# Kernel tuning notes

Hardware: AMD Instinct MI355X
Metric: run time of the kernel (lower is better)

The kernel has to match this reference:

```python
import jax, jax.numpy as jnp
import numpy as np

P = 64       # number of pathways
NV = 512     # features per pathway (nvar[i])
W = 256      # hidden width per pathway
COV = 16     # covariates
B = 2048     # batch
EPS = 1e-5   # BatchNorm eps
SLOPE = 0.2  # LeakyReLU negative slope


def _lrelu(v):
    return jnp.where(v >= 0, v, SLOPE * v)


def setup_inputs() -> dict:
    key = jax.random.key(0)
    ks = jax.random.split(key, 8)
    x = jax.random.normal(ks[0], (B, P * NV + COV), dtype=jnp.float32)
    # per-pathway weights (no bias), stacked across pathways -> grouped GEMM
    W1 = jax.random.normal(ks[1], (P, NV, W), dtype=jnp.float32) * (1.0 / np.sqrt(NV))
    W2 = jax.random.normal(ks[2], (P, W, W), dtype=jnp.float32) * (1.0 / np.sqrt(W))
    W3 = jax.random.normal(ks[3], (P, W), dtype=jnp.float32) * (1.0 / np.sqrt(W))
    gamma = jnp.ones((P,), dtype=jnp.float32)   # bn_path weight
    beta = jnp.zeros((P,), dtype=jnp.float32)   # bn_path bias
    fc_w = jax.random.normal(ks[4], (P + COV, 1), dtype=jnp.float32) * 0.05
    fc_b = jnp.full((1,), 0.001, dtype=jnp.float32)
    return {"x": x, "W1": W1, "W2": W2, "W3": W3,
            "gamma": gamma, "beta": beta, "fc_w": fc_w, "fc_b": fc_b}


def reference(x, W1, W2, W3, gamma, beta, fc_w, fc_b):
    # pathway blocks (dropout = identity in eval): grouped GEMMs over P pathways
    xp = x[:, : P * NV].reshape(B, P, NV)
    h = _lrelu(jnp.einsum('bpi,pio->bpo', xp, W1))
    h = _lrelu(jnp.einsum('bpi,pio->bpo', h, W2))
    p = _lrelu(jnp.einsum('bpi,pi->bp', h, W3))          # [B, P]
    # BatchNorm1d (training-mode batch statistics, biased variance)
    mean = p.mean(axis=0)
    var = p.var(axis=0)
    pn = (p - mean) / jnp.sqrt(var + EPS) * gamma + beta
    # global L2 (Frobenius) normalization, as torch.norm(pathway_layer, 2)
    pn = pn / jnp.linalg.norm(pn)
    # concat covariates, final linear + sigmoid
    z = jnp.concatenate([pn, x[:, P * NV: P * NV + COV]], axis=1)  # [B, P+COV]
    return jax.nn.sigmoid(z @ fc_w + fc_b)                         # [B, 1]
```

## Files before the change

### kernel.cpp

```cpp
#include <hip/hip_runtime.h>
#include <hip/hip_bf16.h>

#define PW 64
#define NV 512
#define HW 256
#define COV 16
#define BATCH 2048
#define XROW (PW * NV + COV)
#define IMG 16384
#define IMG2 8192

typedef short s16x8 __attribute__((ext_vector_type(8)));
typedef float f32x4 __attribute__((ext_vector_type(4)));

__device__ __forceinline__ unsigned short f2bf(float f) {
    union { float f; unsigned int u; } v;
    v.f = f;
    unsigned int u = v.u;
    unsigned int r = (u + 0x7fffu + ((u >> 16) & 1u)) >> 16;
    return (unsigned short)r;
}

__device__ __forceinline__ unsigned int pack2(float a, float b) {
    __hip_bfloat162 h = __float22bfloat162_rn(float2{a, b});
    union { __hip_bfloat162 h; unsigned int u; } c;
    c.h = h;
    return c.u;
}

__device__ __forceinline__ float lrelu(float v) { return v >= 0.f ? v : 0.2f * v; }

__device__ __forceinline__ void gl_lds16(const void* g, void* l) {
    __builtin_amdgcn_global_load_lds(
        (const __attribute__((address_space(1))) void*)g,
        (__attribute__((address_space(3))) void*)l, 16, 0, 0);
}

#define WAITV(n) asm volatile("s_waitcnt vmcnt(" #n ") lgkmcnt(0)" ::: "memory")
#define BAR()    __builtin_amdgcn_s_barrier()
#define SCHED0() __builtin_amdgcn_sched_barrier(0)

__global__ __launch_bounds__(256)
void transpose_all(const float* __restrict__ W1, const float* __restrict__ W2,
                   unsigned short* __restrict__ W1I, unsigned short* __restrict__ W2I) {
    __shared__ float tile[64][260];
    int bx = blockIdx.x;
    const int t = threadIdx.x;
    const bool isW1 = bx < 512;
    const float* src;
    if (isW1) {
        int p = bx >> 3, kb = bx & 7;
        src = W1 + ((size_t)p * NV + kb * 64) * HW;
    } else {
        int b2 = bx - 512;
        int p = b2 >> 2, kb64 = b2 & 3;
        src = W2 + ((size_t)p * HW + kb64 * 64) * HW;
    }
    #pragma unroll
    for (int i = 0; i < 16; ++i) {
        int idx = t + i * 256;
        int r = idx >> 6, c4 = (idx & 63) << 2;
        *(float4*)&tile[r][c4] = *(const float4*)(src + (size_t)r * HW + c4);
    }
    __syncthreads();
    if (isW1) {
        int p = bx >> 3, kb = bx & 7;
        unsigned short* dst = W1I + (size_t)(p * 8 + kb) * IMG;
        #pragma unroll
        for (int pass = 0; pass < 8; ++pass) {
            int idx = pass * 256 + t;
            int n = idx >> 3, s = idx & 7;
            int g = s ^ (n & 7);
            unsigned short v[8];
            #pragma unroll
            for (int j = 0; j < 8; ++j)
                v[j] = f2bf(tile[g * 8 + j][n]);
            *(s16x8*)(dst + (size_t)idx * 8) = *(s16x8*)v;
        }
    } else {
        int b2 = bx - 512;
        int p = b2 >> 2, kb64 = b2 & 3;
        unsigned short* dst = W2I + (size_t)(p * 8 + kb64 * 2) * IMG2;
        #pragma unroll
        for (int pass = 0; pass < 8; ++pass) {
            int idx = pass * 256 + t;
            int h = idx >> 10;
            int rem = idx & 1023;
            int n = rem >> 2, s = rem & 3;
            int g = s ^ ((n >> 1) & 3);
            int krow = h * 32 + g * 8;
            unsigned short v[8];
            #pragma unroll
            for (int j = 0; j < 8; ++j)
                v[j] = f2bf(tile[krow + j][n]);
            *(s16x8*)(dst + (size_t)h * IMG2 + n * 32 + s * 8) = *(s16x8*)v;
        }
    }
}

__global__ __launch_bounds__(256, 2)
void pathway_fused(const float* __restrict__ x, const unsigned short* __restrict__ W1I,
                   const unsigned short* __restrict__ W2I, const float* __restrict__ W3,
                   float* __restrict__ pvec) {
    __shared__ __align__(16) unsigned short lds[40960];

    const int lin = blockIdx.x;
    const int xcd = lin & 7;
    const int idx = lin >> 3;
    const int p   = xcd * 8 + (idx >> 5);
    const int m   = idx & 31;
    const int bm0 = m * 64;

    const int t = threadIdx.x;
    const int lane = t & 63;
    const int wave = t >> 6;
    const int wn   = wave * 64;
    const int l15  = lane & 15;
    const int quad = lane >> 4;

    const float* Ap          = x   + (size_t)p * NV;
    const unsigned short* B1 = W1I + (size_t)p * 8 * IMG;
    const unsigned short* B2 = W2I + (size_t)p * 8 * IMG2;

    int arow[4], aoff[4];
    #pragma unroll
    for (int i = 0; i < 4; ++i) {
        int ii = t + i * 256;
        arow[i] = ii >> 4;
        int acol = (ii & 15) * 4;
        int slot = (acol >> 3) ^ (arow[i] & 7);
        aoff[i] = arow[i] * 64 + slot * 8 + (acol & 7);
    }
    int acolc[4];
    #pragma unroll
    for (int i = 0; i < 4; ++i) acolc[i] = ((t + i * 256) & 15) * 4;

    float4 S0[4], S1[4];
    f32x4 acc[4][4] = {};

#define XLOAD(dst, k0) { \
    _Pragma("unroll") \
    for (int i = 0; i < 4; ++i) \
        dst[i] = *(const float4*)(Ap + (size_t)(bm0 + arow[i]) * XROW + (k0) + acolc[i]); }

#define APACK(src, buf) { \
    unsigned short* Asb = lds + 32768 + (buf) * 4096; \
    _Pragma("unroll") \
    for (int i = 0; i < 4; ++i) { \
        uint2 u; \
        u.x = pack2(src[i].x, src[i].y); \
        u.y = pack2(src[i].z, src[i].w); \
        *(uint2*)&Asb[aoff[i]] = u; } }

#define B1STAGE(buf, kb) { \
    const unsigned short* img = B1 + (size_t)(kb) * IMG; \
    _Pragma("unroll") \
    for (int c = 0; c < 8; ++c) { \
        int off = wave * 8192 + c * 1024; \
        gl_lds16((const char*)img + off + lane * 16, (char*)lds + (buf) * 32768 + off); } }

#define MFMA_A(buf) { \
    const unsigned short* Asb = lds + 32768 + (buf) * 4096; \
    const unsigned short* Bsb = lds + (buf) * 16384; \
    __builtin_amdgcn_s_setprio(1); \
    _Pragma("unroll") \
    for (int kk = 0; kk < 64; kk += 32) { \
        s16x8 af[4], bfr[4]; \
        _Pragma("unroll") \
        for (int mi = 0; mi < 4; ++mi) { \
            int row = mi * 16 + l15; \
            int slot = ((kk >> 3) + quad) ^ (row & 7); \
            af[mi] = *(const s16x8*)&Asb[row * 64 + slot * 8]; } \
        _Pragma("unroll") \
        for (int ni = 0; ni < 4; ++ni) { \
            int row = wn + ni * 16 + l15; \
            int slot = ((kk >> 3) + quad) ^ (row & 7); \
            bfr[ni] = *(const s16x8*)&Bsb[row * 64 + slot * 8]; } \
        _Pragma("unroll") \
        for (int mi = 0; mi < 4; ++mi) \
            _Pragma("unroll") \
            for (int ni = 0; ni < 4; ++ni) \
                acc[mi][ni] = __builtin_amdgcn_mfma_f32_16x16x32_bf16( \
                    af[mi], bfr[ni], acc[mi][ni], 0, 0, 0); } \
    __builtin_amdgcn_s_setprio(0); }

#define W2STAGE(buf, kb) { \
    const unsigned short* img = B2 + (size_t)(kb) * IMG2; \
    _Pragma("unroll") \
    for (int c = 0; c < 4; ++c) { \
        int off = wave * 4096 + c * 1024; \
        gl_lds16((const char*)img + off + lane * 16, (char*)lds + 16384 + (buf) * 8192 + off); } }

#define MFMA_B(buf, kb) { \
    const unsigned short* W2b = lds + 16384 + (buf) * 8192; \
    __builtin_amdgcn_s_setprio(1); \
    { \
        s16x8 af[4], bfr[4]; \
        _Pragma("unroll") \
        for (int mi = 0; mi < 4; ++mi) { \
            int row = mi * 16 + l15; \
            int slot = ((kb) * 4 + quad) ^ (row & 7); \
            af[mi] = *(const s16x8*)&lds[row * 256 + slot * 8]; } \
        _Pragma("unroll") \
        for (int ni = 0; ni < 4; ++ni) { \
            int row = wn + ni * 16 + l15; \
            int slot = quad ^ ((row >> 1) & 3); \
            bfr[ni] = *(const s16x8*)&W2b[row * 32 + slot * 8]; } \
        _Pragma("unroll") \
        for (int mi = 0; mi < 4; ++mi) \
            _Pragma("unroll") \
            for (int ni = 0; ni < 4; ++ni) \
                acc[mi][ni] = __builtin_amdgcn_mfma_f32_16x16x32_bf16( \
                    af[mi], bfr[ni], acc[mi][ni], 0, 0, 0); \
    } \
    __builtin_amdgcn_s_setprio(0); }

#define STEP_A(tt, sLoad, sPack, WN) { \
    if ((tt) + 1 < 8) B1STAGE(1 - ((tt) & 1), (tt) + 1); \
    SCHED0(); \
    if ((tt) + 2 < 8) XLOAD(sLoad, ((tt) + 2) * 64); \
    if ((tt) + 1 < 8) APACK(sPack, 1 - ((tt) & 1)); \
    MFMA_A((tt) & 1); \
    WAITV(WN); \
    BAR(); \
    SCHED0(); }

#define STEP_B(tt, WN) { \
    if ((tt) + 2 < 8) W2STAGE(((tt) + 2) % 3, (tt) + 2); \
    SCHED0(); \
    MFMA_B((tt) % 3, (tt)); \
    WAITV(WN); \
    BAR(); \
    SCHED0(); }

    XLOAD(S0, 0);
    SCHED0();
    B1STAGE(0, 0);
    SCHED0();
    XLOAD(S1, 64);
    APACK(S0, 0);
    WAITV(4);
    BAR();
    SCHED0();

    STEP_A(0, S0, S1, 4);
    STEP_A(1, S1, S0, 4);
    STEP_A(2, S0, S1, 4);
    STEP_A(3, S1, S0, 4);
    STEP_A(4, S0, S1, 4);
    STEP_A(5, S1, S0, 4);
    STEP_A(6, S0, S1, 0);
    STEP_A(7, S1, S0, 0);

    W2STAGE(0, 0);
    SCHED0();
    W2STAGE(1, 1);
    #pragma unroll
    for (int mi = 0; mi < 4; ++mi)
        #pragma unroll
        for (int ni = 0; ni < 4; ++ni)
            #pragma unroll
            for (int r = 0; r < 4; ++r) {
                int row = mi * 16 + quad * 4 + r;
                int col = wn + ni * 16 + l15;
                int slot = (col >> 3) ^ (row & 7);
                lds[row * 256 + slot * 8 + (col & 7)] = f2bf(lrelu(acc[mi][ni][r]));
            }
    WAITV(4);
    BAR();
    SCHED0();

    #pragma unroll
    for (int mi = 0; mi < 4; ++mi)
        #pragma unroll
        for (int ni = 0; ni < 4; ++ni)
            acc[mi][ni] = (f32x4){0.f, 0.f, 0.f, 0.f};

    STEP_B(0, 4);
    STEP_B(1, 4);
    STEP_B(2, 4);
    STEP_B(3, 4);
    STEP_B(4, 4);
    STEP_B(5, 4);
    STEP_B(6, 0);
    STEP_B(7, 0);

    float* red = (float*)(lds + 16384);
    float w3v[4];
    #pragma unroll
    for (int ni = 0; ni < 4; ++ni)
        w3v[ni] = W3[(size_t)p * HW + wn + ni * 16 + l15];
    float part[4][4];
    #pragma unroll
    for (int mi = 0; mi < 4; ++mi) {
        #pragma unroll
        for (int r = 0; r < 4; ++r) {
            float s = 0.f;
            #pragma unroll
            for (int ni = 0; ni < 4; ++ni)
                s += lrelu(acc[mi][ni][r]) * w3v[ni];
            part[mi][r] = s;
        }
    }
    #pragma unroll
    for (int off = 1; off < 16; off <<= 1)
        #pragma unroll
        for (int mi = 0; mi < 4; ++mi)
            #pragma unroll
            for (int r = 0; r < 4; ++r)
                part[mi][r] += __shfl_xor(part[mi][r], off);
    if (l15 == 0)
        #pragma unroll
        for (int mi = 0; mi < 4; ++mi)
            #pragma unroll
            for (int r = 0; r < 4; ++r)
                red[wave * 64 + mi * 16 + quad * 4 + r] = part[mi][r];
    __syncthreads();
    if (t < 64) {
        float s = red[0 * 64 + t] + red[1 * 64 + t] + red[2 * 64 + t] + red[3 * 64 + t];
        pvec[(size_t)p * BATCH + bm0 + t] = lrelu(s);
    }
#undef XLOAD
#undef APACK
#undef B1STAGE
#undef MFMA_A
#undef W2STAGE
#undef MFMA_B
#undef STEP_A
#undef STEP_B
}

__global__ __launch_bounds__(256)
void stats_k(const float* __restrict__ pvec, float* __restrict__ stat) {
    const int p = blockIdx.x;
    float s = 0.f, q = 0.f;
    for (int i = threadIdx.x; i < BATCH; i += 256) {
        float v = pvec[(size_t)p * BATCH + i];
        s += v; q += v * v;
    }
    #pragma unroll
    for (int off = 32; off; off >>= 1) {
        s += __shfl_down(s, off);
        q += __shfl_down(q, off);
    }
    __shared__ float ls[4], lq[4];
    const int wave = threadIdx.x >> 6, lane = threadIdx.x & 63;
    if (lane == 0) { ls[wave] = s; lq[wave] = q; }
    __syncthreads();
    if (threadIdx.x == 0) {
        float S = ls[0] + ls[1] + ls[2] + ls[3];
        float Q = lq[0] + lq[1] + lq[2] + lq[3];
        float mean = S * (1.f / BATCH);
        float var  = Q * (1.f / BATCH) - mean * mean;
        stat[p]       = mean;
        stat[64 + p]  = rsqrtf(var + 1e-5f);
        stat[128 + p] = var;
    }
}

__global__ __launch_bounds__(256)
void final_k(const float* __restrict__ pvec, const float* __restrict__ stat,
             const float* __restrict__ gamma, const float* __restrict__ beta,
             const float* __restrict__ x, const float* __restrict__ fc_w,
             const float* __restrict__ fc_b, float* __restrict__ out) {
    const int b = blockIdx.x * 256 + threadIdx.x;
    float nsq = 0.f;
    #pragma unroll
    for (int p = 0; p < PW; ++p) {
        float g = gamma[p], bt = beta[p], var = stat[128 + p], inv = stat[64 + p];
        nsq += (float)BATCH * (g * g * var * inv * inv + bt * bt);
    }
    const float rn = rsqrtf(nsq);
    float acc = fc_b[0];
    #pragma unroll
    for (int p = 0; p < PW; ++p) {
        float pn = (pvec[(size_t)p * BATCH + b] - stat[p]) * stat[64 + p] * gamma[p] + beta[p];
        acc += pn * rn * fc_w[p];
    }
    #pragma unroll
    for (int c = 0; c < COV; ++c)
        acc += x[(size_t)b * XROW + PW * NV + c] * fc_w[PW + c];
    out[b] = 1.f / (1.f + __expf(-acc));
}

extern "C" void kernel_launch(void* const* d_in, const int* in_sizes, int n_in,
                              void* d_out, int out_size, void* d_ws, size_t ws_size,
                              hipStream_t stream) {
    const float* x     = (const float*)d_in[0];
    const float* W1    = (const float*)d_in[1];
    const float* W2    = (const float*)d_in[2];
    const float* W3    = (const float*)d_in[3];
    const float* gamma = (const float*)d_in[4];
    const float* beta  = (const float*)d_in[5];
    const float* fc_w  = (const float*)d_in[6];
    const float* fc_b  = (const float*)d_in[7];
    float* out = (float*)d_out;

    char* ws = (char*)d_ws;
    size_t off = 0;
    unsigned short* W1I = (unsigned short*)(ws + off); off += (size_t)PW * NV * HW * 2;
    unsigned short* W2I = (unsigned short*)(ws + off); off += (size_t)PW * HW * HW * 2;
    float* pvec = (float*)(ws + off); off += (size_t)PW * BATCH * 4;
    float* stat = (float*)(ws + off); off += 256 * 4;

    transpose_all<<<dim3(512 + 256), 256, 0, stream>>>(W1, W2, W1I, W2I);
    pathway_fused<<<dim3(2048), 256, 0, stream>>>(x, W1I, W2I, W3, pvec);
    stats_k<<<PW, 256, 0, stream>>>(pvec, stat);
    final_k<<<BATCH / 256, 256, 0, stream>>>(pvec, stat, gamma, beta, x, fc_w, fc_b, out);
}
```

Baseline: 481.1 us.

## Enlarge pathway block tile to 256 batch rows with eight waves

Each block of the fused pathway kernel now covers 256 batch rows with 512 threads arranged as 2x4 waves, instead of 64 rows with 4 waves. Every staged W1/W2 tile is reused across four times as many rows, cutting weight traffic into LDS by a factor of four, and the grid shrinks to 512 blocks. LDS use grows to about 160KB, which limits residency to one block per CU. The W2 pipeline also drops from triple to double buffering with a full wait each step, which may expose more load latency.

```diff
diff --git a/kernel.cpp b/kernel.cpp
--- a/kernel.cpp
+++ b/kernel.cpp
@@ -98,23 +98,24 @@
     }
 }
 
-__global__ __launch_bounds__(256, 2)
+__global__ __launch_bounds__(512, 2)
 void pathway_fused(const float* __restrict__ x, const unsigned short* __restrict__ W1I,
                    const unsigned short* __restrict__ W2I, const float* __restrict__ W3,
                    float* __restrict__ pvec) {
-    __shared__ __align__(16) unsigned short lds[40960];
+    __shared__ __align__(16) unsigned short lds[81920];
 
     const int lin = blockIdx.x;
     const int xcd = lin & 7;
     const int idx = lin >> 3;
-    const int p   = xcd * 8 + (idx >> 5);
-    const int m   = idx & 31;
-    const int bm0 = m * 64;
+    const int p   = xcd * 8 + (idx >> 3);
+    const int mt  = idx & 7;
+    const int bm0 = mt * 256;
 
     const int t = threadIdx.x;
     const int lane = t & 63;
     const int wave = t >> 6;
-    const int wn   = wave * 64;
+    const int wm   = wave >> 2;
+    const int wn   = wave & 3;
     const int l15  = lane & 15;
     const int quad = lane >> 4;
 
@@ -122,62 +123,60 @@
     const unsigned short* B1 = W1I + (size_t)p * 8 * IMG;
     const unsigned short* B2 = W2I + (size_t)p * 8 * IMG2;
 
-    int arow[4], aoff[4];
-    #pragma unroll
-    for (int i = 0; i < 4; ++i) {
-        int ii = t + i * 256;
-        arow[i] = ii >> 4;
-        int acol = (ii & 15) * 4;
-        int slot = (acol >> 3) ^ (arow[i] & 7);
-        aoff[i] = arow[i] * 64 + slot * 8 + (acol & 7);
-    }
-    int acolc[4];
-    #pragma unroll
-    for (int i = 0; i < 4; ++i) acolc[i] = ((t + i * 256) & 15) * 4;
-
-    float4 S0[4], S1[4];
-    f32x4 acc[4][4] = {};
-
-#define XLOAD(dst, k0) { \
+    int arow[8], acolc[8], aoff[8];
+    #pragma unroll
+    for (int i = 0; i < 8; ++i) {
+        int ii = t + i * 512;
+        arow[i]  = ii >> 4;
+        acolc[i] = (ii & 15) * 4;
+        int slot = (acolc[i] >> 3) ^ (arow[i] & 7);
+        aoff[i]  = arow[i] * 64 + slot * 8 + (acolc[i] & 7);
+    }
+
+    float4 S[8];
+    f32x4 acc[8][4] = {};
+
+#define XLOAD(k0) { \
     _Pragma("unroll") \
-    for (int i = 0; i < 4; ++i) \
-        dst[i] = *(const float4*)(Ap + (size_t)(bm0 + arow[i]) * XROW + (k0) + acolc[i]); }
-
-#define APACK(src, buf) { \
-    unsigned short* Asb = lds + 32768 + (buf) * 4096; \
+    for (int i = 0; i < 8; ++i) \
+        S[i] = *(const float4*)(Ap + (size_t)(bm0 + arow[i]) * XROW + (k0) + acolc[i]); }
+
+#define APACK(buf) { \
+    unsigned short* Asb = lds + (buf) * 16384; \
     _Pragma("unroll") \
-    for (int i = 0; i < 4; ++i) { \
+    for (int i = 0; i < 8; ++i) { \
         uint2 u; \
-        u.x = pack2(src[i].x, src[i].y); \
-        u.y = pack2(src[i].z, src[i].w); \
+        u.x = pack2(S[i].x, S[i].y); \
+        u.y = pack2(S[i].z, S[i].w); \
         *(uint2*)&Asb[aoff[i]] = u; } }
 
 #define B1STAGE(buf, kb) { \
     const unsigned short* img = B1 + (size_t)(kb) * IMG; \
     _Pragma("unroll") \
-    for (int c = 0; c < 8; ++c) { \
-        int off = wave * 8192 + c * 1024; \
-        gl_lds16((const char*)img + off + lane * 16, (char*)lds + (buf) * 32768 + off); } }
+    for (int c = 0; c < 4; ++c) { \
+        int off = wave * 4096 + c * 1024; \
+        gl_lds16((const char*)img + off + lane * 16, \
+                 (char*)lds + 65536 + (buf) * 32768 + off); } }
 
 #define MFMA_A(buf) { \
-    const unsigned short* Asb = lds + 32768 + (buf) * 4096; \
-    const unsigned short* Bsb = lds + (buf) * 16384; \
+    const unsigned short* Asb = lds + (buf) * 16384; \
+    const unsigned short* Bsb = lds + 32768 + (buf) * 16384; \
     __builtin_amdgcn_s_setprio(1); \
     _Pragma("unroll") \
     for (int kk = 0; kk < 64; kk += 32) { \
-        s16x8 af[4], bfr[4]; \
-        _Pragma("unroll") \
-        for (int mi = 0; mi < 4; ++mi) { \
-            int row = mi * 16 + l15; \
+        s16x8 af[8], bfr[4]; \
+        _Pragma("unroll") \
+        for (int mi = 0; mi < 8; ++mi) { \
+            int row = wm * 128 + mi * 16 + l15; \
             int slot = ((kk >> 3) + quad) ^ (row & 7); \
             af[mi] = *(const s16x8*)&Asb[row * 64 + slot * 8]; } \
         _Pragma("unroll") \
         for (int ni = 0; ni < 4; ++ni) { \
-            int row = wn + ni * 16 + l15; \
+            int row = wn * 64 + ni * 16 + l15; \
             int slot = ((kk >> 3) + quad) ^ (row & 7); \
             bfr[ni] = *(const s16x8*)&Bsb[row * 64 + slot * 8]; } \
         _Pragma("unroll") \
-        for (int mi = 0; mi < 4; ++mi) \
+        for (int mi = 0; mi < 8; ++mi) \
             _Pragma("unroll") \
             for (int ni = 0; ni < 4; ++ni) \
                 acc[mi][ni] = __builtin_amdgcn_mfma_f32_16x16x32_bf16( \
@@ -187,27 +186,28 @@
 #define W2STAGE(buf, kb) { \
     const unsigned short* img = B2 + (size_t)(kb) * IMG2; \
     _Pragma("unroll") \
-    for (int c = 0; c < 4; ++c) { \
-        int off = wave * 4096 + c * 1024; \
-        gl_lds16((const char*)img + off + lane * 16, (char*)lds + 16384 + (buf) * 8192 + off); } }
+    for (int c = 0; c < 2; ++c) { \
+        int off = wave * 2048 + c * 1024; \
+        gl_lds16((const char*)img + off + lane * 16, \
+                 (char*)lds + 131072 + (buf) * 16384 + off); } }
 
 #define MFMA_B(buf, kb) { \
-    const unsigned short* W2b = lds + 16384 + (buf) * 8192; \
+    const unsigned short* W2b = lds + 65536 + (buf) * 8192; \
     __builtin_amdgcn_s_setprio(1); \
     { \
-        s16x8 af[4], bfr[4]; \
-        _Pragma("unroll") \
-        for (int mi = 0; mi < 4; ++mi) { \
-            int row = mi * 16 + l15; \
+        s16x8 af[8], bfr[4]; \
+        _Pragma("unroll") \
+        for (int mi = 0; mi < 8; ++mi) { \
+            int row = wm * 128 + mi * 16 + l15; \
             int slot = ((kb) * 4 + quad) ^ (row & 7); \
             af[mi] = *(const s16x8*)&lds[row * 256 + slot * 8]; } \
         _Pragma("unroll") \
         for (int ni = 0; ni < 4; ++ni) { \
-            int row = wn + ni * 16 + l15; \
+            int row = wn * 64 + ni * 16 + l15; \
             int slot = quad ^ ((row >> 1) & 3); \
             bfr[ni] = *(const s16x8*)&W2b[row * 32 + slot * 8]; } \
         _Pragma("unroll") \
-        for (int mi = 0; mi < 4; ++mi) \
+        for (int mi = 0; mi < 8; ++mi) \
             _Pragma("unroll") \
             for (int ni = 0; ni < 4; ++ni) \
                 acc[mi][ni] = __builtin_amdgcn_mfma_f32_16x16x32_bf16( \
@@ -215,84 +215,84 @@
     } \
     __builtin_amdgcn_s_setprio(0); }
 
-#define STEP_A(tt, sLoad, sPack, WN) { \
+#define STEP_A(tt, WN) { \
     if ((tt) + 1 < 8) B1STAGE(1 - ((tt) & 1), (tt) + 1); \
     SCHED0(); \
-    if ((tt) + 2 < 8) XLOAD(sLoad, ((tt) + 2) * 64); \
-    if ((tt) + 1 < 8) APACK(sPack, 1 - ((tt) & 1)); \
+    if ((tt) + 1 < 8) APACK(1 - ((tt) & 1)); \
+    if ((tt) + 2 < 8) XLOAD(((tt) + 2) * 64); \
+    SCHED0(); \
     MFMA_A((tt) & 1); \
     WAITV(WN); \
     BAR(); \
     SCHED0(); }
 
-#define STEP_B(tt, WN) { \
-    if ((tt) + 2 < 8) W2STAGE(((tt) + 2) % 3, (tt) + 2); \
+#define STEP_B(tt) { \
+    if ((tt) + 1 < 8) W2STAGE(1 - ((tt) & 1), (tt) + 1); \
     SCHED0(); \
-    MFMA_B((tt) % 3, (tt)); \
-    WAITV(WN); \
+    MFMA_B((tt) & 1, (tt)); \
+    WAITV(0); \
     BAR(); \
     SCHED0(); }
 
-    XLOAD(S0, 0);
+    XLOAD(0);
     SCHED0();
     B1STAGE(0, 0);
     SCHED0();
-    XLOAD(S1, 64);
-    APACK(S0, 0);
-    WAITV(4);
+    APACK(0);
+    XLOAD(64);
+    WAITV(8);
     BAR();
     SCHED0();
 
-    STEP_A(0, S0, S1, 4);
-    STEP_A(1, S1, S0, 4);
-    STEP_A(2, S0, S1, 4);
-    STEP_A(3, S1, S0, 4);
-    STEP_A(4, S0, S1, 4);
-    STEP_A(5, S1, S0, 4);
-    STEP_A(6, S0, S1, 0);
-    STEP_A(7, S1, S0, 0);
+    STEP_A(0, 8);
+    STEP_A(1, 8);
+    STEP_A(2, 8);
+    STEP_A(3, 8);
+    STEP_A(4, 8);
+    STEP_A(5, 8);
+    STEP_A(6, 0);
+    STEP_A(7, 0);
 
     W2STAGE(0, 0);
     SCHED0();
-    W2STAGE(1, 1);
-    #pragma unroll
-    for (int mi = 0; mi < 4; ++mi)
+    #pragma unroll
+    for (int mi = 0; mi < 8; ++mi)
         #pragma unroll
         for (int ni = 0; ni < 4; ++ni)
             #pragma unroll
             for (int r = 0; r < 4; ++r) {
-                int row = mi * 16 + quad * 4 + r;
-                int col = wn + ni * 16 + l15;
+                int row = wm * 128 + mi * 16 + quad * 4 + r;
+                int col = wn * 64 + ni * 16 + l15;
                 int slot = (col >> 3) ^ (row & 7);
                 lds[row * 256 + slot * 8 + (col & 7)] = f2bf(lrelu(acc[mi][ni][r]));
             }
-    WAITV(4);
+    WAITV(0);
     BAR();
     SCHED0();
 
     #pragma unroll
-    for (int mi = 0; mi < 4; ++mi)
+    for (int mi = 0; mi < 8; ++mi)
         #pragma unroll
         for (int ni = 0; ni < 4; ++ni)
             acc[mi][ni] = (f32x4){0.f, 0.f, 0.f, 0.f};
 
-    STEP_B(0, 4);
-    STEP_B(1, 4);
-    STEP_B(2, 4);
-    STEP_B(3, 4);
-    STEP_B(4, 4);
-    STEP_B(5, 4);
-    STEP_B(6, 0);
-    STEP_B(7, 0);
-
-    float* red = (float*)(lds + 16384);
+    STEP_B(0);
+    STEP_B(1);
+    STEP_B(2);
+    STEP_B(3);
+    STEP_B(4);
+    STEP_B(5);
+    STEP_B(6);
+    STEP_B(7);
+
+    float* red = (float*)lds;
     float w3v[4];
     #pragma unroll
     for (int ni = 0; ni < 4; ++ni)
-        w3v[ni] = W3[(size_t)p * HW + wn + ni * 16 + l15];
-    float part[4][4];
-    #pragma unroll
-    for (int mi = 0; mi < 4; ++mi) {
+        w3v[ni] = W3[(size_t)p * HW + wn * 64 + ni * 16 + l15];
+    float part[8][4];
+    #pragma unroll
+    for (int mi = 0; mi < 8; ++mi) {
         #pragma unroll
         for (int r = 0; r < 4; ++r) {
             float s = 0.f;
@@ -305,19 +305,19 @@
     #pragma unroll
     for (int off = 1; off < 16; off <<= 1)
         #pragma unroll
-        for (int mi = 0; mi < 4; ++mi)
+        for (int mi = 0; mi < 8; ++mi)
             #pragma unroll
             for (int r = 0; r < 4; ++r)
                 part[mi][r] += __shfl_xor(part[mi][r], off);
     if (l15 == 0)
         #pragma unroll
-        for (int mi = 0; mi < 4; ++mi)
+        for (int mi = 0; mi < 8; ++mi)
             #pragma unroll
             for (int r = 0; r < 4; ++r)
-                red[wave * 64 + mi * 16 + quad * 4 + r] = part[mi][r];
+                red[wn * 256 + wm * 128 + mi * 16 + quad * 4 + r] = part[mi][r];
     __syncthreads();
-    if (t < 64) {
-        float s = red[0 * 64 + t] + red[1 * 64 + t] + red[2 * 64 + t] + red[3 * 64 + t];
+    if (t < 256) {
+        float s = red[0 * 256 + t] + red[1 * 256 + t] + red[2 * 256 + t] + red[3 * 256 + t];
         pvec[(size_t)p * BATCH + bm0 + t] = lrelu(s);
     }
 #undef XLOAD
@@ -404,7 +404,7 @@
     float* stat = (float*)(ws + off); off += 256 * 4;
 
     transpose_all<<<dim3(512 + 256), 256, 0, stream>>>(W1, W2, W1I, W2I);
-    pathway_fused<<<dim3(2048), 256, 0, stream>>>(x, W1I, W2I, W3, pvec);
+    pathway_fused<<<dim3(512), 512, 0, stream>>>(x, W1I, W2I, W3, pvec);
     stats_k<<<PW, 256, 0, stream>>>(pvec, stat);
     final_k<<<BATCH / 256, 256, 0, stream>>>(pvec, stat, gamma, beta, x, fc_w, fc_b, out);
 }
```

Measured after the change: 455.8 us. -5.3%, faster.
